# Kernel optimization log

Measured on AMD Instinct MI355X. Metric: run time of the kernel, lower is better.

## Reference

```python
import jax, jax.numpy as jnp
import numpy as np

DIM = 256
HEADS = 4
DH = 64
B, N, H, W, G = 1, 6, 64, 64, 8
QLEN = H * W
SCALE = DH ** -0.5
EPS = 1e-5


def _ln(x, g, b):
    m = x.mean(-1, keepdims=True)
    v = ((x - m) ** 2).mean(-1, keepdims=True)
    return (x - m) / jnp.sqrt(v + EPS) * g + b


def setup_inputs() -> dict:
    key = jax.random.key(0)
    ks = jax.random.split(key, 16)
    hd = HEADS * DH
    p = lambda k, shp: 0.02 * jax.random.normal(k, shp, dtype=jnp.float32)
    inp = {
        'q': jax.random.normal(ks[0], (B, N, DIM, H, W), dtype=jnp.float32),
        'k': jax.random.normal(ks[1], (B, N, QLEN, G, DIM), dtype=jnp.float32),
        'v': jax.random.normal(ks[2], (B, N, QLEN, G, DIM), dtype=jnp.float32),
        'skip': jax.random.normal(ks[3], (B, DIM, H, W), dtype=jnp.float32),
        'mask': jax.random.randint(ks[4], (B, N, QLEN, 1), 0, 2).astype(bool),
        'ln_q_g': jnp.ones((DIM,), jnp.float32), 'ln_q_b': jnp.zeros((DIM,), jnp.float32),
        'wq': p(ks[5], (DIM, hd)), 'bq': jnp.zeros((hd,), jnp.float32),
        'ln_k_g': jnp.ones((DIM,), jnp.float32), 'ln_k_b': jnp.zeros((DIM,), jnp.float32),
        'wk': p(ks[6], (DIM, hd)), 'bk': jnp.zeros((hd,), jnp.float32),
        'ln_v_g': jnp.ones((DIM,), jnp.float32), 'ln_v_b': jnp.zeros((DIM,), jnp.float32),
        'wv': p(ks[7], (DIM, hd)), 'bv': jnp.zeros((hd,), jnp.float32),
        'w_proj': p(ks[8], (hd, DIM)), 'b_proj': jnp.zeros((DIM,), jnp.float32),
        'ln_pre_g': jnp.ones((DIM,), jnp.float32), 'ln_pre_b': jnp.zeros((DIM,), jnp.float32),
        'w_mlp1': p(ks[9], (DIM, 2 * DIM)), 'b_mlp1': jnp.zeros((2 * DIM,), jnp.float32),
        'w_mlp2': p(ks[10], (2 * DIM, DIM)), 'b_mlp2': jnp.zeros((DIM,), jnp.float32),
        'ln_post_g': jnp.ones((DIM,), jnp.float32), 'ln_post_b': jnp.zeros((DIM,), jnp.float32),
    }
    return inp


def reference(q, k, v, skip, mask,
              ln_q_g, ln_q_b, wq, bq,
              ln_k_g, ln_k_b, wk, bk,
              ln_v_g, ln_v_b, wv, bv,
              w_proj, b_proj,
              ln_pre_g, ln_pre_b,
              w_mlp1, b_mlp1, w_mlp2, b_mlp2,
              ln_post_g, ln_post_b):
    b, n, d, Hh, Ww = q.shape
    g = k.shape[-2]
    Qn = Hh * Ww
    # b n d H W -> b n (H W) d
    qx = jnp.transpose(q, (0, 1, 3, 4, 2)).reshape(b, n, Qn, d)
    qp = _ln(qx, ln_q_g, ln_q_b) @ wq + bq            # (b, n, Q, m*dh)
    kp = _ln(k, ln_k_g, ln_k_b) @ wk + bk             # (b, n, Q, g, m*dh)
    vp = _ln(v, ln_v_g, ln_v_b) @ wv + bv             # (b, n, Q, g, m*dh)
    qh = qp.reshape(b, n, Qn, HEADS, DH)
    kh = kp.reshape(b, n, Qn, g, HEADS, DH)
    # scores: (b, m, Q, n, g)
    dot = SCALE * jnp.einsum('bnqmd,bnqgmd->bmqng', qh, kh)
    mb = jnp.transpose(mask[..., 0], (0, 2, 1))[:, None, :, :, None]  # (b,1,Q,n,1)
    dot = jnp.where(mb, dot, jnp.float32(-1e9))
    att = jax.nn.softmax(dot.reshape(b, HEADS, Qn, n * g), axis=-1)
    vh = vp.reshape(b, n, Qn, g, HEADS, DH)
    vh = jnp.transpose(vh, (0, 4, 2, 1, 3, 5)).reshape(b, HEADS, Qn, n * g, DH)
    a = jnp.einsum('bmqk,bmqkd->bmqd', att, vh)       # (b, m, Q, dh)
    a = jnp.transpose(a, (0, 2, 1, 3)).reshape(b, Qn, HEADS * DH)
    z = a @ w_proj + b_proj
    z = z + jnp.transpose(skip, (0, 2, 3, 1)).reshape(b, Qn, d)
    z = _ln(z, ln_pre_g, ln_pre_b)
    h = jax.nn.gelu(z @ w_mlp1 + b_mlp1, approximate=False) @ w_mlp2 + b_mlp2
    z = _ln(z + h, ln_post_g, ln_post_b)
    return jnp.transpose(z.reshape(b, Hh, Ww, d), (0, 3, 1, 2))
```

## Files before the change

kernel.cpp:

```cpp
#include <hip/hip_runtime.h>
#include <hip/hip_bf16.h>
#include <math.h>

#define NF 6
#define QL 4096
#define SCALE 0.125f
#define EPSLN 1e-5f

typedef __bf16 bf16x8 __attribute__((ext_vector_type(8)));
typedef __bf16 bf16x4 __attribute__((ext_vector_type(4)));
typedef float  f32x4  __attribute__((ext_vector_type(4)));

#define OFF_WQT   0u
#define OFF_WKT   131072u
#define OFF_WVT   262144u
#define OFF_WPT   393216u
#define OFF_W1T   524288u
#define OFF_W2T   786432u
#define OFF_QH    1048576u
#define OFF_ATT   13631488u
#define OFF_OPART 16777216u

__device__ __forceinline__ unsigned short f2bf(float x) {
  union { float f; unsigned u; } v; v.f = x;
  unsigned r = v.u + 0x7FFFu + ((v.u >> 16) & 1u);
  return (unsigned short)(r >> 16);
}
__device__ __forceinline__ unsigned long long pack4bf(float a, float b, float c, float d) {
  unsigned d0 = (unsigned)f2bf(a) | ((unsigned)f2bf(b) << 16);
  unsigned d1 = (unsigned)f2bf(c) | ((unsigned)f2bf(d) << 16);
  return (unsigned long long)d0 | ((unsigned long long)d1 << 32);
}
__device__ __forceinline__ void async_copy16(const float* g, float* l) {
  __builtin_amdgcn_global_load_lds(
      (const __attribute__((address_space(1))) unsigned int*)g,
      (__attribute__((address_space(3))) unsigned int*)l, 16, 0, 0);
}

__global__ void __launch_bounds__(256)
prep_kernel(const float* __restrict__ wq, const float* __restrict__ wk,
            const float* __restrict__ wv, const float* __restrict__ wp,
            const float* __restrict__ w1, const float* __restrict__ w2,
            unsigned short* __restrict__ wsu16)
{
  const int blk = blockIdx.x, t = threadIdx.x;
  const float* src; unsigned short* dst; int N, KT, ntile;
  if (blk < 64) {
    int mi = blk >> 4; ntile = blk & 15; N = 256; KT = 8;
    src = (mi == 0) ? wq : (mi == 1) ? wk : (mi == 2) ? wv : wp;
    dst = wsu16 + (size_t)mi * 65536;
  } else if (blk < 96) {
    ntile = blk - 64; N = 512; KT = 8; src = w1; dst = wsu16 + OFF_W1T / 2;
  } else {
    ntile = blk - 96; N = 256; KT = 16; src = w2; dst = wsu16 + OFF_W2T / 2;
  }
  const int lane = t & 63;
  const int lr = lane & 15, quad = lane >> 4;
  const int ncol = ntile * 16 + lr;
  for (int kt = (t >> 6); kt < KT; kt += 4) {
    unsigned v8[8];
#pragma unroll
    for (int j = 0; j < 8; ++j) {
      int krow = kt * 32 + quad * 8 + j;
      v8[j] = f2bf(src[(size_t)krow * N + ncol]);
    }
    uint4 u;
    u.x = v8[0] | (v8[1] << 16); u.y = v8[2] | (v8[3] << 16);
    u.z = v8[4] | (v8[5] << 16); u.w = v8[6] | (v8[7] << 16);
    *(uint4*)(dst + ((size_t)(ntile * KT + kt) * 512 + lane * 8)) = u;
  }
}

__global__ void __launch_bounds__(256, 4)
projq_kernel(const float* __restrict__ src,
             const float* __restrict__ lng, const float* __restrict__ lnb,
             const unsigned short* __restrict__ wTp,
             const float* __restrict__ bias,
             unsigned short* __restrict__ qh)
{
  __shared__ __align__(16) unsigned short s_x[64 * 264];
  const int t = threadIdx.x, blk = blockIdx.x;
  const int n = blk >> 6, qp0 = (blk & 63) << 6;

  {
    const int l16 = t & 15, dg = t >> 4;
    for (int it = 0; it < 16; ++it) {
      int dcol = it * 16 + dg;
      float4 x = *(const float4*)(src + ((size_t)(n * 256 + dcol)) * 4096 + qp0 + l16 * 4);
      s_x[(l16 * 4 + 0) * 264 + dcol] = f2bf(x.x);
      s_x[(l16 * 4 + 1) * 264 + dcol] = f2bf(x.y);
      s_x[(l16 * 4 + 2) * 264 + dcol] = f2bf(x.z);
      s_x[(l16 * 4 + 3) * 264 + dcol] = f2bf(x.w);
    }
  }
  __syncthreads();
  {
    const int row = t >> 2, sl = t & 3;
    float s = 0.f, s2 = 0.f;
#pragma unroll
    for (int i = 0; i < 8; ++i) {
      bf16x8 xv = *(const bf16x8*)(s_x + row * 264 + (i * 4 + sl) * 8);
#pragma unroll
      for (int j = 0; j < 8; ++j) { float f = (float)xv[j]; s += f; s2 += f * f; }
    }
    s += __shfl_xor(s, 1, 64);  s += __shfl_xor(s, 2, 64);
    s2 += __shfl_xor(s2, 1, 64); s2 += __shfl_xor(s2, 2, 64);
    float mu = s * (1.f / 256.f);
    float var = s2 * (1.f / 256.f) - mu * mu;
    float istd = rsqrtf(var + EPSLN);
#pragma unroll
    for (int i = 0; i < 8; ++i) {
      int c = (i * 4 + sl) * 8;
      bf16x8 xv = *(const bf16x8*)(s_x + row * 264 + c);
      f32x4 ga = *(const f32x4*)(lng + c), gb = *(const f32x4*)(lng + c + 4);
      f32x4 ba = *(const f32x4*)(lnb + c), bb = *(const f32x4*)(lnb + c + 4);
      uint4 u;
      u.x = (unsigned)f2bf(((float)xv[0] - mu) * istd * ga[0] + ba[0]) |
            ((unsigned)f2bf(((float)xv[1] - mu) * istd * ga[1] + ba[1]) << 16);
      u.y = (unsigned)f2bf(((float)xv[2] - mu) * istd * ga[2] + ba[2]) |
            ((unsigned)f2bf(((float)xv[3] - mu) * istd * ga[3] + ba[3]) << 16);
      u.z = (unsigned)f2bf(((float)xv[4] - mu) * istd * gb[0] + bb[0]) |
            ((unsigned)f2bf(((float)xv[5] - mu) * istd * gb[1] + bb[1]) << 16);
      u.w = (unsigned)f2bf(((float)xv[6] - mu) * istd * gb[2] + bb[2]) |
            ((unsigned)f2bf(((float)xv[7] - mu) * istd * gb[3] + bb[3]) << 16);
      *(uint4*)(s_x + row * 264 + c) = u;
    }
  }
  __syncthreads();

  const int w = t >> 6, lane = t & 63, lr = lane & 15, quad = lane >> 4;
  f32x4 acc[4][4];
  {
    f32x4 z = {0.f, 0.f, 0.f, 0.f};
#pragma unroll
    for (int a = 0; a < 4; ++a)
#pragma unroll
      for (int b = 0; b < 4; ++b) acc[a][b] = z;
  }
  for (int kt = 0; kt < 8; ++kt) {
    bf16x8 xf[4];
#pragma unroll
    for (int mt = 0; mt < 4; ++mt)
      xf[mt] = *(const bf16x8*)(s_x + (mt * 16 + lr) * 264 + kt * 32 + quad * 8);
#pragma unroll
    for (int nt = 0; nt < 4; ++nt) {
      bf16x8 wf = *(const bf16x8*)(wTp + ((size_t)((w * 4 + nt) * 8 + kt) * 512 + lane * 8));
#pragma unroll
      for (int mt = 0; mt < 4; ++mt)
        acc[nt][mt] = __builtin_amdgcn_mfma_f32_16x16x32_bf16(wf, xf[mt], acc[nt][mt], 0, 0, 0);
    }
  }
  __syncthreads();
#pragma unroll
  for (int nt = 0; nt < 4; ++nt) {
    int n0 = w * 64 + nt * 16 + quad * 4;
    f32x4 bb = *(const f32x4*)(bias + n0);
#pragma unroll
    for (int mt = 0; mt < 4; ++mt) {
      int m = mt * 16 + lr;
      f32x4 a = acc[nt][mt];
      *(unsigned long long*)(s_x + m * 264 + n0) =
          pack4bf(a[0] + bb[0], a[1] + bb[1], a[2] + bb[2], a[3] + bb[3]);
    }
  }
  __syncthreads();
  unsigned char* ob = (unsigned char*)qh + ((size_t)n * QL + qp0) * 512;
#pragma unroll
  for (int i = 0; i < 8; ++i) {
    int lin = i * 4096 + t * 16;
    int r = lin >> 9, off = lin & 511;
    *(uint4*)(ob + lin) = *(const uint4*)((const unsigned char*)s_x + r * 528 + off);
  }
}

__global__ void __launch_bounds__(256, 3)
projkv_kernel(const float* __restrict__ src,
              const float* __restrict__ lng, const float* __restrict__ lnb,
              const unsigned short* __restrict__ wTp,
              const float* __restrict__ bias,
              const unsigned short* __restrict__ qh,
              float* __restrict__ attg,
              float* __restrict__ opart,
              int kind)
{
  __shared__ __align__(16) float s_raw[32 * 272];
  __shared__ __align__(16) unsigned short s_x[32 * 264];
  const int t = threadIdx.x, blk = blockIdx.x;
  const int n = blk >> 10, qp0 = (blk & 1023) << 2;
  const int w = t >> 6, lane = t & 63;

  {
    const float* gb = src + (size_t)blk * 32 * 256 + lane * 4;
    float* lb = s_raw + (w * 8) * 272;
#pragma unroll
    for (int i = 0; i < 8; ++i)
      async_copy16(gb + (size_t)(w * 8 + i) * 256, lb + i * 272);
  }
  __syncthreads();

  {
    const int row = t >> 3, sl = t & 7;
    float s = 0.f, s2 = 0.f;
#pragma unroll
    for (int i = 0; i < 8; ++i) {
      f32x4 x = *(const f32x4*)(s_raw + row * 272 + sl * 4 + i * 32);
      s  += x[0] + x[1] + x[2] + x[3];
      s2 += x[0] * x[0] + x[1] * x[1] + x[2] * x[2] + x[3] * x[3];
    }
    s += __shfl_xor(s, 1, 64);  s += __shfl_xor(s, 2, 64);  s += __shfl_xor(s, 4, 64);
    s2 += __shfl_xor(s2, 1, 64); s2 += __shfl_xor(s2, 2, 64); s2 += __shfl_xor(s2, 4, 64);
    float mu = s * (1.f / 256.f);
    float var = s2 * (1.f / 256.f) - mu * mu;
    float istd = rsqrtf(var + EPSLN);
#pragma unroll
    for (int i = 0; i < 8; ++i) {
      int c = sl * 4 + i * 32;
      f32x4 x = *(const f32x4*)(s_raw + row * 272 + c);
      f32x4 g = *(const f32x4*)(lng + c);
      f32x4 b = *(const f32x4*)(lnb + c);
      *(unsigned long long*)(s_x + row * 264 + c) =
          pack4bf((x[0] - mu) * istd * g[0] + b[0], (x[1] - mu) * istd * g[1] + b[1],
                  (x[2] - mu) * istd * g[2] + b[2], (x[3] - mu) * istd * g[3] + b[3]);
    }
  }
  __syncthreads();

  const int lr = lane & 15, quad = lane >> 4;
  f32x4 acc[4][2];
  {
    f32x4 z = {0.f, 0.f, 0.f, 0.f};
#pragma unroll
    for (int a = 0; a < 4; ++a) { acc[a][0] = z; acc[a][1] = z; }
  }
  for (int kt = 0; kt < 8; ++kt) {
    bf16x8 xf[2];
    xf[0] = *(const bf16x8*)(s_x + lr * 264 + kt * 32 + quad * 8);
    xf[1] = *(const bf16x8*)(s_x + (16 + lr) * 264 + kt * 32 + quad * 8);
#pragma unroll
    for (int nt = 0; nt < 4; ++nt) {
      bf16x8 wf = *(const bf16x8*)(wTp + ((size_t)((w * 4 + nt) * 8 + kt) * 512 + lane * 8));
      acc[nt][0] = __builtin_amdgcn_mfma_f32_16x16x32_bf16(wf, xf[0], acc[nt][0], 0, 0, 0);
      acc[nt][1] = __builtin_amdgcn_mfma_f32_16x16x32_bf16(wf, xf[1], acc[nt][1], 0, 0, 0);
    }
  }
  __syncthreads();
#pragma unroll
  for (int nt = 0; nt < 4; ++nt) {
    int n0 = w * 64 + nt * 16 + quad * 4;
    f32x4 bb = *(const f32x4*)(bias + n0);
#pragma unroll
    for (int mt = 0; mt < 2; ++mt) {
      int m = mt * 16 + lr;
      f32x4 a = acc[nt][mt];
      *(unsigned long long*)(s_x + m * 264 + n0) =
          pack4bf(a[0] + bb[0], a[1] + bb[1], a[2] + bb[2], a[3] + bb[3]);
    }
  }
  __syncthreads();

  if (kind == 0) {
    if (t < 128) {
      const int p = t >> 5, m = (t >> 3) & 3, g = t & 7;
      const unsigned short* kr = s_x + (p * 8 + g) * 264 + m * 64;
      const unsigned short* qr = qh + ((size_t)n * QL + qp0 + p) * 256 + m * 64;
      float dot = 0.f;
#pragma unroll
      for (int i = 0; i < 8; ++i) {
        bf16x8 kv = *(const bf16x8*)(kr + i * 8);
        bf16x8 qv = *(const bf16x8*)(qr + i * 8);
#pragma unroll
        for (int j = 0; j < 8; ++j) dot += (float)kv[j] * (float)qv[j];
      }
      attg[(((size_t)(qp0 + p)) * 4 + m) * 48 + n * 8 + g] = dot * SCALE;
    }
  } else {
    const int p = t >> 6, c0 = (t & 63) * 4, m = c0 >> 6;
    const float* ar = attg + (((size_t)(qp0 + p)) * 4 + m) * 48 + n * 8;
    f32x4 a0 = *(const f32x4*)ar, a1 = *(const f32x4*)(ar + 4);
    float aw[8] = {a0[0], a0[1], a0[2], a0[3], a1[0], a1[1], a1[2], a1[3]};
    float o[4] = {0.f, 0.f, 0.f, 0.f};
#pragma unroll
    for (int g = 0; g < 8; ++g) {
      bf16x4 vv = *(const bf16x4*)(s_x + (p * 8 + g) * 264 + c0);
#pragma unroll
      for (int j = 0; j < 4; ++j) o[j] += aw[g] * (float)vv[j];
    }
    f32x4 ov = {o[0], o[1], o[2], o[3]};
    *(f32x4*)(opart + ((size_t)n * QL + qp0 + p) * 256 + c0) = ov;
  }
}

__global__ void __launch_bounds__(256)
softmax_kernel(float* __restrict__ attg, const int* __restrict__ mask)
{
  const int tg = blockIdx.x * 256 + threadIdx.x;
  const int p = tg >> 2;
  float* row = attg + (size_t)tg * 48;
  float xs[48];
#pragma unroll
  for (int i = 0; i < 12; ++i) {
    float4 x = ((const float4*)row)[i];
    xs[4 * i] = x.x; xs[4 * i + 1] = x.y; xs[4 * i + 2] = x.z; xs[4 * i + 3] = x.w;
  }
#pragma unroll
  for (int n = 0; n < 6; ++n) {
    if (!mask[n * QL + p]) {
#pragma unroll
      for (int j = 0; j < 8; ++j) xs[n * 8 + j] = -1e9f;
    }
  }
  float mx = -3.0e38f;
#pragma unroll
  for (int i = 0; i < 48; ++i) mx = fmaxf(mx, xs[i]);
  float sm = 0.f;
#pragma unroll
  for (int i = 0; i < 48; ++i) { float e = __expf(xs[i] - mx); xs[i] = e; sm += e; }
  float inv = 1.f / sm;
#pragma unroll
  for (int i = 0; i < 12; ++i)
    ((float4*)row)[i] = make_float4(xs[4 * i] * inv, xs[4 * i + 1] * inv,
                                    xs[4 * i + 2] * inv, xs[4 * i + 3] * inv);
}

__global__ void __launch_bounds__(256)
epi_kernel(const float* __restrict__ opart, const float* __restrict__ skip,
           const unsigned short* __restrict__ wpp, const float* __restrict__ bp,
           const float* __restrict__ lng1, const float* __restrict__ lnb1,
           const unsigned short* __restrict__ w1p, const float* __restrict__ b1,
           const unsigned short* __restrict__ w2p, const float* __restrict__ b2,
           const float* __restrict__ lng2, const float* __restrict__ lnb2,
           float* __restrict__ out)
{
  __shared__ __align__(16) unsigned char smem[50688];
  unsigned short* s_a  = (unsigned short*)smem;
  float*          s_z  = (float*)(smem + 8448);
  unsigned short* s_zb = (unsigned short*)(smem + 25344);
  unsigned short* s_h  = (unsigned short*)(smem + 33792);
  float*          s_z2 = (float*)(smem + 33792);
  const int t = threadIdx.x, q0 = blockIdx.x * 16;

#pragma unroll
  for (int i = 0; i < 4; ++i) {
    int pos = i * 256 + t, p = pos >> 6, c4 = (pos & 63) * 4;
    const float* base = opart + (size_t)(q0 + p) * 256 + c4;
    f32x4 s = {0.f, 0.f, 0.f, 0.f};
#pragma unroll
    for (int nn = 0; nn < 6; ++nn) s += *(const f32x4*)(base + (size_t)nn * QL * 256);
    *(unsigned long long*)(s_a + p * 264 + c4) = pack4bf(s[0], s[1], s[2], s[3]);
  }
  __syncthreads();

  const int w = t >> 6, lane = t & 63, lr = lane & 15, quad = lane >> 4;

  {
    f32x4 acc[4];
    f32x4 z = {0.f, 0.f, 0.f, 0.f};
#pragma unroll
    for (int a = 0; a < 4; ++a) acc[a] = z;
    for (int kt = 0; kt < 8; ++kt) {
      bf16x8 xf = *(const bf16x8*)(s_a + lr * 264 + kt * 32 + quad * 8);
#pragma unroll
      for (int nt = 0; nt < 4; ++nt) {
        bf16x8 wf = *(const bf16x8*)(wpp + ((size_t)((w * 4 + nt) * 8 + kt) * 512 + lane * 8));
        acc[nt] = __builtin_amdgcn_mfma_f32_16x16x32_bf16(wf, xf, acc[nt], 0, 0, 0);
      }
    }
#pragma unroll
    for (int nt = 0; nt < 4; ++nt) {
      int n0 = w * 64 + nt * 16 + quad * 4;
      f32x4 bb = *(const f32x4*)(bp + n0);
      f32x4 sk;
#pragma unroll
      for (int j = 0; j < 4; ++j) sk[j] = skip[(size_t)(n0 + j) * QL + q0 + lr];
      *(f32x4*)(s_z + lr * 264 + n0) = acc[nt] + bb + sk;
    }
  }
  __syncthreads();

  {
    int r = t >> 4, l = t & 15;
    float s = 0.f, s2 = 0.f;
#pragma unroll
    for (int i = 0; i < 16; ++i) {
      float x = s_z[r * 264 + l + 16 * i];
      s += x; s2 += x * x;
    }
    s += __shfl_xor(s, 1, 64); s += __shfl_xor(s, 2, 64);
    s += __shfl_xor(s, 4, 64); s += __shfl_xor(s, 8, 64);
    s2 += __shfl_xor(s2, 1, 64); s2 += __shfl_xor(s2, 2, 64);
    s2 += __shfl_xor(s2, 4, 64); s2 += __shfl_xor(s2, 8, 64);
    float mu = s * (1.f / 256.f);
    float var = s2 * (1.f / 256.f) - mu * mu;
    float istd = rsqrtf(var + EPSLN);
#pragma unroll
    for (int i = 0; i < 16; ++i) {
      int d = l + 16 * i;
      float nv = (s_z[r * 264 + d] - mu) * istd * lng1[d] + lnb1[d];
      s_z[r * 264 + d] = nv;
      s_zb[r * 264 + d] = f2bf(nv);
    }
  }
  __syncthreads();

  {
    f32x4 acc[8];
    f32x4 z = {0.f, 0.f, 0.f, 0.f};
#pragma unroll
    for (int a = 0; a < 8; ++a) acc[a] = z;
    for (int kt = 0; kt < 8; ++kt) {
      bf16x8 xf = *(const bf16x8*)(s_zb + lr * 264 + kt * 32 + quad * 8);
#pragma unroll
      for (int nt = 0; nt < 8; ++nt) {
        bf16x8 wf = *(const bf16x8*)(w1p + ((size_t)((w * 8 + nt) * 8 + kt) * 512 + lane * 8));
        acc[nt] = __builtin_amdgcn_mfma_f32_16x16x32_bf16(wf, xf, acc[nt], 0, 0, 0);
      }
    }
#pragma unroll
    for (int nt = 0; nt < 8; ++nt) {
      int n0 = w * 128 + nt * 16 + quad * 4;
      f32x4 bb = *(const f32x4*)(b1 + n0);
      float hv[4];
#pragma unroll
      for (int j = 0; j < 4; ++j) {
        float val = acc[nt][j] + bb[j];
        hv[j] = 0.5f * val * (1.f + erff(val * 0.70710678118654752f));
      }
      *(unsigned long long*)(s_h + lr * 528 + n0) = pack4bf(hv[0], hv[1], hv[2], hv[3]);
    }
  }
  __syncthreads();

  {
    f32x4 acc[4];
    f32x4 z = {0.f, 0.f, 0.f, 0.f};
#pragma unroll
    for (int a = 0; a < 4; ++a) acc[a] = z;
    for (int kt = 0; kt < 16; ++kt) {
      bf16x8 xf = *(const bf16x8*)(s_h + lr * 528 + kt * 32 + quad * 8);
#pragma unroll
      for (int nt = 0; nt < 4; ++nt) {
        bf16x8 wf = *(const bf16x8*)(w2p + ((size_t)((w * 4 + nt) * 16 + kt) * 512 + lane * 8));
        acc[nt] = __builtin_amdgcn_mfma_f32_16x16x32_bf16(wf, xf, acc[nt], 0, 0, 0);
      }
    }
    f32x4 res[4];
#pragma unroll
    for (int nt = 0; nt < 4; ++nt) {
      int n0 = w * 64 + nt * 16 + quad * 4;
      f32x4 bb = *(const f32x4*)(b2 + n0);
      f32x4 zr = *(const f32x4*)(s_z + lr * 264 + n0);
      res[nt] = acc[nt] + bb + zr;
    }
    __syncthreads();
#pragma unroll
    for (int nt = 0; nt < 4; ++nt) {
      int n0 = w * 64 + nt * 16 + quad * 4;
      *(f32x4*)(s_z2 + lr * 264 + n0) = res[nt];
    }
  }
  __syncthreads();

  {
    int r = t >> 4, l = t & 15;
    float s = 0.f, s2 = 0.f;
#pragma unroll
    for (int i = 0; i < 16; ++i) {
      float x = s_z2[r * 264 + l + 16 * i];
      s += x; s2 += x * x;
    }
    s += __shfl_xor(s, 1, 64); s += __shfl_xor(s, 2, 64);
    s += __shfl_xor(s, 4, 64); s += __shfl_xor(s, 8, 64);
    s2 += __shfl_xor(s2, 1, 64); s2 += __shfl_xor(s2, 2, 64);
    s2 += __shfl_xor(s2, 4, 64); s2 += __shfl_xor(s2, 8, 64);
    float mu = s * (1.f / 256.f);
    float var = s2 * (1.f / 256.f) - mu * mu;
    float istd = rsqrtf(var + EPSLN);
#pragma unroll
    for (int i = 0; i < 16; ++i) {
      int d = l + 16 * i;
      s_z2[r * 264 + d] = (s_z2[r * 264 + d] - mu) * istd * lng2[d] + lnb2[d];
    }
  }
  __syncthreads();

#pragma unroll
  for (int i = 0; i < 16; ++i) {
    int c = i * 16 + (t >> 4), p = t & 15;
    out[(size_t)c * QL + q0 + p] = s_z2[p * 264 + c];
  }
}

extern "C" void kernel_launch(void* const* d_in, const int* in_sizes, int n_in,
                              void* d_out, int out_size, void* d_ws, size_t ws_size,
                              hipStream_t stream) {
  (void)in_sizes; (void)n_in; (void)out_size; (void)ws_size;
  const float* q     = (const float*)d_in[0];
  const float* k     = (const float*)d_in[1];
  const float* v     = (const float*)d_in[2];
  const float* skip  = (const float*)d_in[3];
  const int*   mask  = (const int*)d_in[4];
  const float* lnqg  = (const float*)d_in[5];
  const float* lnqb  = (const float*)d_in[6];
  const float* wq    = (const float*)d_in[7];
  const float* bq    = (const float*)d_in[8];
  const float* lnkg  = (const float*)d_in[9];
  const float* lnkb  = (const float*)d_in[10];
  const float* wk    = (const float*)d_in[11];
  const float* bk    = (const float*)d_in[12];
  const float* lnvg  = (const float*)d_in[13];
  const float* lnvb  = (const float*)d_in[14];
  const float* wv    = (const float*)d_in[15];
  const float* bv    = (const float*)d_in[16];
  const float* wp    = (const float*)d_in[17];
  const float* bp    = (const float*)d_in[18];
  const float* lng1  = (const float*)d_in[19];
  const float* lnb1  = (const float*)d_in[20];
  const float* w1    = (const float*)d_in[21];
  const float* b1    = (const float*)d_in[22];
  const float* w2    = (const float*)d_in[23];
  const float* b2    = (const float*)d_in[24];
  const float* lng2  = (const float*)d_in[25];
  const float* lnb2  = (const float*)d_in[26];
  float* out = (float*)d_out;

  unsigned char* ws = (unsigned char*)d_ws;
  unsigned short* wsu16 = (unsigned short*)d_ws;
  unsigned short* wqT = (unsigned short*)(ws + OFF_WQT);
  unsigned short* wkT = (unsigned short*)(ws + OFF_WKT);
  unsigned short* wvT = (unsigned short*)(ws + OFF_WVT);
  unsigned short* wpT = (unsigned short*)(ws + OFF_WPT);
  unsigned short* w1T = (unsigned short*)(ws + OFF_W1T);
  unsigned short* w2T = (unsigned short*)(ws + OFF_W2T);
  unsigned short* qh  = (unsigned short*)(ws + OFF_QH);
  float* attg  = (float*)(ws + OFF_ATT);
  float* opart = (float*)(ws + OFF_OPART);

  hipLaunchKernelGGL(prep_kernel, dim3(112), dim3(256), 0, stream,
                     wq, wk, wv, wp, w1, w2, wsu16);
  hipLaunchKernelGGL(projq_kernel, dim3(384), dim3(256), 0, stream,
                     q, lnqg, lnqb, wqT, bq, qh);
  hipLaunchKernelGGL(projkv_kernel, dim3(6144), dim3(256), 0, stream,
                     k, lnkg, lnkb, wkT, bk, qh, attg, opart, 0);
  hipLaunchKernelGGL(softmax_kernel, dim3(64), dim3(256), 0, stream,
                     attg, mask);
  hipLaunchKernelGGL(projkv_kernel, dim3(6144), dim3(256), 0, stream,
                     v, lnvg, lnvb, wvT, bv, qh, attg, opart, 1);
  hipLaunchKernelGGL(epi_kernel, dim3(QL / 16), dim3(256), 0, stream,
                     opart, skip, wpT, bp, lng1, lnb1, w1T, b1, w2T, b2, lng2, lnb2, out);
}
```

Baseline: 574.6 us.

## Fuse softmax into V projection and load raw rows directly to registers

Removes the standalone softmax kernel. Each V-projection block now recomputes the masked softmax for its 4 pixels into shared memory before the weighted sum. The async global-to-LDS staging buffer is replaced by direct register loads, which frees LDS so the occupancy hint rises from 3 to 4 blocks. The K-dot stage now uses all 256 threads with a shuffle reduction. The cost is that softmax is computed redundantly across the 6 view blocks per pixel, and register pressure goes up.

Result: faster. 555.7 us (-3.3%).

```diff
diff --git a/kernel.cpp b/kernel.cpp
--- a/kernel.cpp
+++ b/kernel.cpp
@@ -30,11 +30,6 @@
   unsigned d0 = (unsigned)f2bf(a) | ((unsigned)f2bf(b) << 16);
   unsigned d1 = (unsigned)f2bf(c) | ((unsigned)f2bf(d) << 16);
   return (unsigned long long)d0 | ((unsigned long long)d1 << 32);
-}
-__device__ __forceinline__ void async_copy16(const float* g, float* l) {
-  __builtin_amdgcn_global_load_lds(
-      (const __attribute__((address_space(1))) unsigned int*)g,
-      (__attribute__((address_space(3))) unsigned int*)l, 16, 0, 0);
 }
 
 __global__ void __launch_bounds__(256)
@@ -173,39 +168,33 @@
   }
 }
 
-__global__ void __launch_bounds__(256, 3)
+__global__ void __launch_bounds__(256, 4)
 projkv_kernel(const float* __restrict__ src,
               const float* __restrict__ lng, const float* __restrict__ lnb,
               const unsigned short* __restrict__ wTp,
               const float* __restrict__ bias,
               const unsigned short* __restrict__ qh,
               float* __restrict__ attg,
+              const int* __restrict__ mask,
               float* __restrict__ opart,
               int kind)
 {
-  __shared__ __align__(16) float s_raw[32 * 272];
   __shared__ __align__(16) unsigned short s_x[32 * 264];
+  __shared__ __align__(16) float s_att[16 * 48];
   const int t = threadIdx.x, blk = blockIdx.x;
   const int n = blk >> 10, qp0 = (blk & 1023) << 2;
   const int w = t >> 6, lane = t & 63;
 
   {
-    const float* gb = src + (size_t)blk * 32 * 256 + lane * 4;
-    float* lb = s_raw + (w * 8) * 272;
-#pragma unroll
-    for (int i = 0; i < 8; ++i)
-      async_copy16(gb + (size_t)(w * 8 + i) * 256, lb + i * 272);
-  }
-  __syncthreads();
-
-  {
     const int row = t >> 3, sl = t & 7;
+    const float* gr = src + ((size_t)blk * 32 + row) * 256 + sl * 4;
+    f32x4 xv[8];
     float s = 0.f, s2 = 0.f;
 #pragma unroll
     for (int i = 0; i < 8; ++i) {
-      f32x4 x = *(const f32x4*)(s_raw + row * 272 + sl * 4 + i * 32);
-      s  += x[0] + x[1] + x[2] + x[3];
-      s2 += x[0] * x[0] + x[1] * x[1] + x[2] * x[2] + x[3] * x[3];
+      xv[i] = *(const f32x4*)(gr + i * 32);
+#pragma unroll
+      for (int j = 0; j < 4; ++j) { float f = xv[i][j]; s += f; s2 += f * f; }
     }
     s += __shfl_xor(s, 1, 64);  s += __shfl_xor(s, 2, 64);  s += __shfl_xor(s, 4, 64);
     s2 += __shfl_xor(s2, 1, 64); s2 += __shfl_xor(s2, 2, 64); s2 += __shfl_xor(s2, 4, 64);
@@ -215,13 +204,44 @@
 #pragma unroll
     for (int i = 0; i < 8; ++i) {
       int c = sl * 4 + i * 32;
-      f32x4 x = *(const f32x4*)(s_raw + row * 272 + c);
       f32x4 g = *(const f32x4*)(lng + c);
       f32x4 b = *(const f32x4*)(lnb + c);
       *(unsigned long long*)(s_x + row * 264 + c) =
-          pack4bf((x[0] - mu) * istd * g[0] + b[0], (x[1] - mu) * istd * g[1] + b[1],
-                  (x[2] - mu) * istd * g[2] + b[2], (x[3] - mu) * istd * g[3] + b[3]);
-    }
+          pack4bf((xv[i][0] - mu) * istd * g[0] + b[0],
+                  (xv[i][1] - mu) * istd * g[1] + b[1],
+                  (xv[i][2] - mu) * istd * g[2] + b[2],
+                  (xv[i][3] - mu) * istd * g[3] + b[3]);
+    }
+  }
+
+  if (kind == 1 && t < 64) {
+    const int r = t >> 2, sl = t & 3;
+    const int p = r >> 2, pix = qp0 + p;
+    const float* ar = attg + (((size_t)pix) * 4 + (r & 3)) * 48 + sl * 12;
+    float x[12];
+#pragma unroll
+    for (int i = 0; i < 3; ++i) {
+      f32x4 v4 = *(const f32x4*)(ar + i * 4);
+      x[i * 4] = v4[0]; x[i * 4 + 1] = v4[1]; x[i * 4 + 2] = v4[2]; x[i * 4 + 3] = v4[3];
+    }
+#pragma unroll
+    for (int i = 0; i < 12; ++i) {
+      int nn = (sl * 12 + i) >> 3;
+      if (!mask[nn * QL + pix]) x[i] = -1e9f;
+    }
+    float mx = -3.0e38f;
+#pragma unroll
+    for (int i = 0; i < 12; ++i) mx = fmaxf(mx, x[i]);
+    mx = fmaxf(mx, __shfl_xor(mx, 1, 64));
+    mx = fmaxf(mx, __shfl_xor(mx, 2, 64));
+    float sm = 0.f;
+#pragma unroll
+    for (int i = 0; i < 12; ++i) { float e = __expf(x[i] - mx); x[i] = e; sm += e; }
+    sm += __shfl_xor(sm, 1, 64);
+    sm += __shfl_xor(sm, 2, 64);
+    float inv = 1.f / sm;
+#pragma unroll
+    for (int i = 0; i < 12; ++i) s_att[r * 48 + sl * 12 + i] = x[i] * inv;
   }
   __syncthreads();
 
@@ -259,25 +279,26 @@
   __syncthreads();
 
   if (kind == 0) {
-    if (t < 128) {
-      const int p = t >> 5, m = (t >> 3) & 3, g = t & 7;
-      const unsigned short* kr = s_x + (p * 8 + g) * 264 + m * 64;
-      const unsigned short* qr = qh + ((size_t)n * QL + qp0 + p) * 256 + m * 64;
-      float dot = 0.f;
-#pragma unroll
-      for (int i = 0; i < 8; ++i) {
-        bf16x8 kv = *(const bf16x8*)(kr + i * 8);
-        bf16x8 qv = *(const bf16x8*)(qr + i * 8);
-#pragma unroll
-        for (int j = 0; j < 8; ++j) dot += (float)kv[j] * (float)qv[j];
-      }
+    const int p = t >> 6, m = (t >> 4) & 3, g = (t >> 1) & 7, h = t & 1;
+    const unsigned short* kr = s_x + (p * 8 + g) * 264 + m * 64 + h * 32;
+    const unsigned short* qr = qh + ((size_t)n * QL + qp0 + p) * 256 + m * 64 + h * 32;
+    float dot = 0.f;
+#pragma unroll
+    for (int i = 0; i < 4; ++i) {
+      bf16x8 kv = *(const bf16x8*)(kr + i * 8);
+      bf16x8 qv = *(const bf16x8*)(qr + i * 8);
+#pragma unroll
+      for (int j = 0; j < 8; ++j) dot += (float)kv[j] * (float)qv[j];
+    }
+    dot += __shfl_xor(dot, 1, 64);
+    if (h == 0)
       attg[(((size_t)(qp0 + p)) * 4 + m) * 48 + n * 8 + g] = dot * SCALE;
-    }
   } else {
     const int p = t >> 6, c0 = (t & 63) * 4, m = c0 >> 6;
-    const float* ar = attg + (((size_t)(qp0 + p)) * 4 + m) * 48 + n * 8;
-    f32x4 a0 = *(const f32x4*)ar, a1 = *(const f32x4*)(ar + 4);
-    float aw[8] = {a0[0], a0[1], a0[2], a0[3], a1[0], a1[1], a1[2], a1[3]};
+    const float* ar = s_att + (p * 4 + m) * 48 + n * 8;
+    float aw[8];
+#pragma unroll
+    for (int j = 0; j < 8; ++j) aw[j] = ar[j];
     float o[4] = {0.f, 0.f, 0.f, 0.f};
 #pragma unroll
     for (int g = 0; g < 8; ++g) {
@@ -288,38 +309,6 @@
     f32x4 ov = {o[0], o[1], o[2], o[3]};
     *(f32x4*)(opart + ((size_t)n * QL + qp0 + p) * 256 + c0) = ov;
   }
-}
-
-__global__ void __launch_bounds__(256)
-softmax_kernel(float* __restrict__ attg, const int* __restrict__ mask)
-{
-  const int tg = blockIdx.x * 256 + threadIdx.x;
-  const int p = tg >> 2;
-  float* row = attg + (size_t)tg * 48;
-  float xs[48];
-#pragma unroll
-  for (int i = 0; i < 12; ++i) {
-    float4 x = ((const float4*)row)[i];
-    xs[4 * i] = x.x; xs[4 * i + 1] = x.y; xs[4 * i + 2] = x.z; xs[4 * i + 3] = x.w;
-  }
-#pragma unroll
-  for (int n = 0; n < 6; ++n) {
-    if (!mask[n * QL + p]) {
-#pragma unroll
-      for (int j = 0; j < 8; ++j) xs[n * 8 + j] = -1e9f;
-    }
-  }
-  float mx = -3.0e38f;
-#pragma unroll
-  for (int i = 0; i < 48; ++i) mx = fmaxf(mx, xs[i]);
-  float sm = 0.f;
-#pragma unroll
-  for (int i = 0; i < 48; ++i) { float e = __expf(xs[i] - mx); xs[i] = e; sm += e; }
-  float inv = 1.f / sm;
-#pragma unroll
-  for (int i = 0; i < 12; ++i)
-    ((float4*)row)[i] = make_float4(xs[4 * i] * inv, xs[4 * i + 1] * inv,
-                                    xs[4 * i + 2] * inv, xs[4 * i + 3] * inv);
 }
 
 __global__ void __launch_bounds__(256)
@@ -540,11 +529,9 @@
   hipLaunchKernelGGL(projq_kernel, dim3(384), dim3(256), 0, stream,
                      q, lnqg, lnqb, wqT, bq, qh);
   hipLaunchKernelGGL(projkv_kernel, dim3(6144), dim3(256), 0, stream,
-                     k, lnkg, lnkb, wkT, bk, qh, attg, opart, 0);
-  hipLaunchKernelGGL(softmax_kernel, dim3(64), dim3(256), 0, stream,
-                     attg, mask);
+                     k, lnkg, lnkb, wkT, bk, qh, attg, mask, opart, 0);
   hipLaunchKernelGGL(projkv_kernel, dim3(6144), dim3(256), 0, stream,
-                     v, lnvg, lnvb, wvT, bv, qh, attg, opart, 1);
+                     v, lnvg, lnvb, wvT, bv, qh, attg, mask, opart, 1);
   hipLaunchKernelGGL(epi_kernel, dim3(QL / 16), dim3(256), 0, stream,
                      opart, skip, wpT, bp, lng1, lnb1, w1T, b1, w2T, b2, lng2, lnb2, out);
 }
```
